# Performance work log

Measured on AMD Instinct MI355X. Metric: run time of the kernel, lower is better.

The kernel has to match this reference:

```python
import jax, jax.numpy as jnp
import numpy as np

EMB, HID, SEQ = 768, 512, 2048
BATCH = 2
EPS = 1e-6
LN_EPS = 1e-5
ROPE_BASE = 10000.0
NEG_BIG = -1e9  # stands in for -inf diagonal mask (identical entmax output, NaN-safe)


def rotate_half(x):
    d = x.shape[-1] // 2
    return jnp.concatenate([-x[..., d:], x[..., :d]], axis=-1)


def rope_tables(L, D, dtype=jnp.float32):
    inv_freq = 1.0 / (ROPE_BASE ** (jnp.arange(0, D, 2, dtype=jnp.float32) / D))
    t = jnp.arange(L, dtype=jnp.float32)
    freqs = jnp.outer(t, inv_freq)            # [L, D/2]
    emb = jnp.concatenate([freqs, freqs], -1)  # [L, D]
    return jnp.cos(emb).astype(dtype), jnp.sin(emb).astype(dtype)


def layernorm(x, gamma, beta):
    mu = jnp.mean(x, axis=-1, keepdims=True)
    var = jnp.mean(jnp.square(x - mu), axis=-1, keepdims=True)
    return (x - mu) * jax.lax.rsqrt(var + LN_EPS) * gamma + beta


def entmax15(z):
    """Exact 1.5-entmax along last axis (Peters & Martins sort algorithm)."""
    z = z / 2.0
    z = z - jnp.max(z, axis=-1, keepdims=True)
    zs = -jnp.sort(-z, axis=-1)                      # descending
    L = z.shape[-1]
    k = jnp.arange(1, L + 1, dtype=z.dtype)
    cum = jnp.cumsum(zs, axis=-1)
    cum2 = jnp.cumsum(zs * zs, axis=-1)
    mean = cum / k
    ss = cum2 - cum * mean                           # k*(E[x^2]-E[x]^2)
    delta = (1.0 - ss) / k
    tau = mean - jnp.sqrt(jnp.maximum(delta, 0.0))
    support = jnp.sum((tau <= zs).astype(jnp.int32), axis=-1)
    tau_star = jnp.take_along_axis(tau, (support - 1)[..., None], axis=-1)
    return jnp.square(jnp.maximum(z - tau_star, 0.0))


def setup_inputs() -> dict:
    key = jax.random.key(0)
    ks = jax.random.split(key, 3)
    x = jax.random.normal(ks[0], (BATCH, SEQ, EMB), dtype=jnp.float32)
    Wq = jax.random.normal(ks[1], (HID, EMB), dtype=jnp.float32) / np.sqrt(EMB)
    Wk = jax.random.normal(ks[2], (HID, EMB), dtype=jnp.float32) / np.sqrt(EMB)
    return {
        "x": x, "Wq": Wq, "Wk": Wk,
        "q_gamma": jnp.ones((HID,), jnp.float32), "q_beta": jnp.zeros((HID,), jnp.float32),
        "k_gamma": jnp.ones((HID,), jnp.float32), "k_beta": jnp.zeros((HID,), jnp.float32),
        "C_weight": jnp.ones((1,), jnp.float32),
        "F_weight": jnp.ones((1,), jnp.float32),
        "S_weight": jnp.ones((1,), jnp.float32),
    }


def reference(x, Wq, Wk, q_gamma, q_beta, k_gamma, k_beta, C_weight, F_weight, S_weight):
    B, L, _ = x.shape
    q = layernorm(x @ Wq.T, q_gamma, q_beta)   # [B,L,D]
    k = layernorm(x @ Wk.T, k_gamma, k_beta)
    cos, sin = rope_tables(L, q.shape[-1], q.dtype)
    q = q * cos + rotate_half(q) * sin
    k = k * cos + rotate_half(k) * sin

    wC = 2.0 * jax.nn.sigmoid(C_weight)
    wF = 2.0 * jax.nn.sigmoid(F_weight)
    wS = 2.0 * jax.nn.sigmoid(S_weight)

    Gkk = jnp.einsum('bld,ble->bde', k, k)     # [B,D,D]
    Gkq = jnp.einsum('bld,ble->bde', k, q)
    Gqq = jnp.einsum('bld,ble->bde', q, q)

    C_raw = jnp.einsum('bid,bde,bje->bij', q, Gkk, q)  # [B,L,L]
    F_raw = jnp.einsum('bid,bde,bje->bij', q, Gkq, k)
    S_raw = jnp.einsum('bid,bde,bje->bij', k, Gqq, k)

    C = C_raw - jnp.mean(C_raw, axis=-1, keepdims=True)
    Fm = F_raw - jnp.mean(F_raw, axis=-1, keepdims=True)
    S = S_raw - jnp.mean(S_raw, axis=-1, keepdims=True)

    pC = jnp.clip(entmax15(wC * C), 0.0, 1.0 - EPS)
    pF = jnp.clip(entmax15(wF * Fm), 0.0, 1.0 - EPS)
    pS = jnp.clip(entmax15(wS * S), 0.0, 1.0 - EPS)

    pC = pC * jax.lax.rsqrt(jnp.sum(pC, axis=-2, keepdims=True) + EPS)
    pS = pS * jax.lax.rsqrt(jnp.sum(pS, axis=-2, keepdims=True) + EPS)

    pC = jnp.maximum((1.0 - 2.0 * EPS) * pC + EPS, EPS)
    pF = jnp.maximum((1.0 - 2.0 * EPS) * pF + EPS, EPS)
    pS = jnp.maximum((1.0 - 2.0 * EPS) * pS + EPS, EPS)

    H = (jnp.log(pC) + jnp.log(pF) + jnp.log(pS)) / 3.0
    diag = jnp.eye(L, dtype=bool)[None]
    H = jnp.where(diag, NEG_BIG, H)
    H = entmax15(H)
    return H, pC, pF, pS
```

## Files before the change

kernel.cpp:

```cpp
#include <hip/hip_runtime.h>
#include <cstddef>
#include <math.h>

#define B_   2
#define L_   2048
#define D_   512
#define E_   768
static const size_t LL   = (size_t)L_ * L_;
static const size_t SLOT = (size_t)B_ * LL;

#define QK_N  ((size_t)B_ * L_ * D_)
#define G1_N  ((size_t)512 * 512)
#define G_N   ((size_t)6 * G1_N)
#define U_N   ((size_t)6 * L_ * D_)
#define X_N   ((size_t)4096 * 768)
#define W_N   ((size_t)512 * 768)

typedef unsigned short u16;
typedef __attribute__((ext_vector_type(8))) _Float16 half8;
typedef __attribute__((ext_vector_type(4))) float f32x4;

__device__ __forceinline__ void split2(float f, u16& h0, u16& h1) {
    _Float16 a = (_Float16)f;
    _Float16 b = (_Float16)((f - (float)a) * 4096.0f);
    h0 = __builtin_bit_cast(u16, a);
    h1 = __builtin_bit_cast(u16, b);
}

typedef const __attribute__((address_space(1))) void gas_void;
typedef __attribute__((address_space(3))) void las_void;

__device__ __forceinline__ void gload16(const u16* g, u16* l) {
    __builtin_amdgcn_global_load_lds((gas_void*)g, (las_void*)l, 16, 0, 0);
}

template<bool PROM>
__device__ __forceinline__ void gemm64g(const u16* __restrict__ Ap, size_t Aps, int lda,
                                        const u16* __restrict__ Bp, size_t Bps, int ldb,
                                        int K, int m0, int n0, int tid,
                                        double outv[2][2][4]) {
    __shared__ u16 SA[2][64][32], SB[2][64][32];
    f32x4 accH[2][2], accM[2][2];
#pragma unroll
    for (int i = 0; i < 2; ++i)
#pragma unroll
        for (int j = 0; j < 2; ++j) {
            accH[i][j] = (f32x4){0.f, 0.f, 0.f, 0.f};
            accM[i][j] = (f32x4){0.f, 0.f, 0.f, 0.f};
        }
    double accD[2][2][4] = {};
    int lane = tid & 63, w = tid >> 6;
    int wm = (w & 1) << 5, wn = (w >> 1) << 5;
    int fr = lane & 15, ko8 = lane >> 4;

    int rb = w << 4;
    int srow = rb + (lane >> 2);
    int schunk = (lane & 3) ^ ((srow >> 1) & 3);

    int nstep = K >> 5;
    for (int s = 0; s < nstep; ++s) {
        int k0 = s << 5;
#pragma unroll
        for (int sp = 0; sp < 2; ++sp) {
            gload16(Ap + (size_t)sp * Aps + (size_t)(m0 + srow) * lda + k0 + (schunk << 3),
                    &SA[sp][rb][0]);
            gload16(Bp + (size_t)sp * Bps + (size_t)(n0 + srow) * ldb + k0 + (schunk << 3),
                    &SB[sp][rb][0]);
        }
        __syncthreads();
        half8 a[2][2], b[2][2];
#pragma unroll
        for (int f = 0; f < 2; ++f) {
            int ra = wm + f * 16 + fr;
            int rbn = wn + f * 16 + fr;
            int ca = (ko8 ^ ((ra >> 1) & 3)) << 3;
            int cb = (ko8 ^ ((rbn >> 1) & 3)) << 3;
#pragma unroll
            for (int sp = 0; sp < 2; ++sp) {
                a[f][sp] = *reinterpret_cast<const half8*>(&SA[sp][ra][ca]);
                b[f][sp] = *reinterpret_cast<const half8*>(&SB[sp][rbn][cb]);
            }
        }
#pragma unroll
        for (int fi = 0; fi < 2; ++fi)
#pragma unroll
            for (int fj = 0; fj < 2; ++fj) {
                accH[fi][fj] = __builtin_amdgcn_mfma_f32_16x16x32_f16(a[fi][0], b[fj][0], accH[fi][fj], 0, 0, 0);
                accM[fi][fj] = __builtin_amdgcn_mfma_f32_16x16x32_f16(a[fi][0], b[fj][1], accM[fi][fj], 0, 0, 0);
                accM[fi][fj] = __builtin_amdgcn_mfma_f32_16x16x32_f16(a[fi][1], b[fj][0], accM[fi][fj], 0, 0, 0);
            }
        __syncthreads();
        if (PROM) {
#pragma unroll
            for (int fi = 0; fi < 2; ++fi)
#pragma unroll
                for (int fj = 0; fj < 2; ++fj) {
#pragma unroll
                    for (int r = 0; r < 4; ++r) accD[fi][fj][r] += (double)accH[fi][fj][r];
                    accH[fi][fj] = (f32x4){0.f, 0.f, 0.f, 0.f};
                }
        }
    }
    const double S1 = 1.0 / 4096.0;
#pragma unroll
    for (int fi = 0; fi < 2; ++fi)
#pragma unroll
        for (int fj = 0; fj < 2; ++fj)
#pragma unroll
            for (int r = 0; r < 4; ++r)
                outv[fi][fj][r] = (PROM ? accD[fi][fj][r] : (double)accH[fi][fj][r])
                                + (double)accM[fi][fj][r] * S1;
}

__device__ __forceinline__ void gstage128(const u16* __restrict__ P, size_t pstride, int ld,
                                          int r0, int k0, int lane, int w,
                                          u16 S[2][128][32]) {
#pragma unroll
    for (int sp = 0; sp < 2; ++sp)
#pragma unroll
        for (int t = 0; t < 2; ++t) {
            int rb = (w << 5) + (t << 4);
            int row = rb + (lane >> 2);
            int chunk = (lane & 3) ^ ((row >> 1) & 3);
            const u16* src = P + (size_t)sp * pstride + (size_t)(r0 + row) * ld
                             + (k0 + (chunk << 3));
            gload16(src, &S[sp][rb][0]);
        }
}

__device__ __forceinline__ void gemm128(const u16* __restrict__ Ap, size_t Aps, int lda,
                                        const u16* __restrict__ Bp, size_t Bps, int ldb,
                                        int K, int m0, int n0, int tid,
                                        float* __restrict__ out, int ldo) {
    __shared__ u16 SA[2][128][32], SB[2][128][32];
    f32x4 accH[4][4], accM[4][4];
#pragma unroll
    for (int i = 0; i < 4; ++i)
#pragma unroll
        for (int j = 0; j < 4; ++j) {
            accH[i][j] = (f32x4){0.f, 0.f, 0.f, 0.f};
            accM[i][j] = (f32x4){0.f, 0.f, 0.f, 0.f};
        }
    int lane = tid & 63, w = tid >> 6;
    int wm = (w & 1) << 6, wn = (w >> 1) << 6;
    int fr = lane & 15, ko8 = lane >> 4;

    int nstep = K >> 5;
    for (int s = 0; s < nstep; ++s) {
        int k0 = s << 5;
        gstage128(Ap, Aps, lda, m0, k0, lane, w, SA);
        gstage128(Bp, Bps, ldb, n0, k0, lane, w, SB);
        __syncthreads();
        half8 a[4][2], b[4][2];
#pragma unroll
        for (int f = 0; f < 4; ++f) {
            int ra = wm + (f << 4) + fr;
            int rbn = wn + (f << 4) + fr;
            int ca = (ko8 ^ ((ra >> 1) & 3)) << 3;
            int cb = (ko8 ^ ((rbn >> 1) & 3)) << 3;
#pragma unroll
            for (int sp = 0; sp < 2; ++sp) {
                a[f][sp] = *reinterpret_cast<const half8*>(&SA[sp][ra][ca]);
                b[f][sp] = *reinterpret_cast<const half8*>(&SB[sp][rbn][cb]);
            }
        }
#pragma unroll
        for (int fi = 0; fi < 4; ++fi)
#pragma unroll
            for (int fj = 0; fj < 4; ++fj) {
                accH[fi][fj] = __builtin_amdgcn_mfma_f32_16x16x32_f16(a[fi][0], b[fj][0], accH[fi][fj], 0, 0, 0);
                accM[fi][fj] = __builtin_amdgcn_mfma_f32_16x16x32_f16(a[fi][0], b[fj][1], accM[fi][fj], 0, 0, 0);
                accM[fi][fj] = __builtin_amdgcn_mfma_f32_16x16x32_f16(a[fi][1], b[fj][0], accM[fi][fj], 0, 0, 0);
            }
        __syncthreads();
    }
    const double S1 = 1.0 / 4096.0;
    int col = lane & 15, rbase = (lane >> 4) << 2;
#pragma unroll
    for (int fi = 0; fi < 4; ++fi)
#pragma unroll
        for (int fj = 0; fj < 4; ++fj)
#pragma unroll
            for (int r = 0; r < 4; ++r) {
                int mm = m0 + wm + (fi << 4) + rbase + r;
                int nn = n0 + wn + (fj << 4) + col;
                out[(size_t)mm * ldo + nn] =
                    (float)((double)accH[fi][fj][r] + (double)accM[fi][fj][r] * S1);
            }
}

__global__ __launch_bounds__(256) void k_prep(const float* __restrict__ x,
                                              const float* __restrict__ Wq,
                                              const float* __restrict__ Wk,
                                              u16* __restrict__ xP,
                                              u16* __restrict__ WP,
                                              double* __restrict__ tg) {
    int bx = blockIdx.x;
    if (bx < L_) {
        int l = bx, j = threadIdx.x;
        double e = (double)j * (1.0 / 256.0);
        double inv = pow(10000.0, -e);
        double ang = (double)l * inv;
        tg[(size_t)l * 512 + j] = cos(ang);
        tg[(size_t)l * 512 + 256 + j] = sin(ang);
        return;
    }
    size_t gid = (size_t)(bx - L_) * 256 + threadIdx.x;
    const size_t XH = X_N / 2, WH = W_N / 2;
    const float* src; u16* dst; size_t pn, off;
    if (gid < XH)            { src = x  + 2 * gid;              dst = xP;            pn = X_N; off = 2 * gid; }
    else if (gid < XH + WH)  { size_t g = gid - XH;      src = Wq + 2 * g; dst = WP;            pn = W_N; off = 2 * g; }
    else                     { size_t g = gid - XH - WH; src = Wk + 2 * g; dst = WP + 2 * W_N;  pn = W_N; off = 2 * g; }
    float2 v = *reinterpret_cast<const float2*>(src);
    u16 a0, a1, b0, b1;
    split2(v.x, a0, a1);
    split2(v.y, b0, b1);
    *reinterpret_cast<unsigned*>(dst + off)      = (unsigned)a0 | ((unsigned)b0 << 16);
    *reinterpret_cast<unsigned*>(dst + pn + off) = (unsigned)a1 | ((unsigned)b1 << 16);
}

__global__ __launch_bounds__(256, 2) void k_proj(const u16* __restrict__ xP,
                                                 const u16* __restrict__ WP,
                                                 float* __restrict__ qraw,
                                                 float* __restrict__ kraw) {
    int z = blockIdx.z;
    float* out = z ? kraw : qraw;
    const u16* Bp = WP + (size_t)z * 2 * W_N;
    gemm128(xP, X_N, E_, Bp, W_N, E_, E_,
            blockIdx.y * 128, blockIdx.x * 128, threadIdx.x, out, D_);
}

__global__ __launch_bounds__(256) void k_lnrope(const float* __restrict__ qraw,
                                                const float* __restrict__ kraw,
                                                const double* __restrict__ tg,
                                                const float* __restrict__ qg, const float* __restrict__ qb,
                                                const float* __restrict__ kg, const float* __restrict__ kb,
                                                u16* __restrict__ qP, u16* __restrict__ kP) {
    int row = blockIdx.x;
    int l = row & (L_ - 1);
    int tid = threadIdx.x;
    int half = tid >> 7, t = tid & 127;
    __shared__ double nrow[2][D_];
    __shared__ double red[8];
    __shared__ double cs_[256], sn_[256];
    {
        int j = tid & 255;
        if (tid < 256) { cs_[j] = tg[(size_t)l * 512 + j]; sn_[j] = tg[(size_t)l * 512 + 256 + j]; }
    }
    const float* rp = (half ? kraw : qraw) + (size_t)row * D_;
    const float* g  = half ? kg : qg;
    const float* bt = half ? kb : qb;
    u16* P = half ? kP : qP;
    float4 v = reinterpret_cast<const float4*>(rp)[t];
    double vv[4] = {(double)v.x, (double)v.y, (double)v.z, (double)v.w};
    double s = vv[0] + vv[1] + vv[2] + vv[3];
    double s2 = vv[0]*vv[0] + vv[1]*vv[1] + vv[2]*vv[2] + vv[3]*vv[3];
    for (int off = 32; off; off >>= 1) { s += __shfl_xor(s, off); s2 += __shfl_xor(s2, off); }
    int wv = tid >> 6;
    if ((tid & 63) == 0) { red[wv * 2] = s; red[wv * 2 + 1] = s2; }
    __syncthreads();
    double mu  = (red[half * 4 + 0] + red[half * 4 + 2]) * (1.0 / D_);
    double var = (red[half * 4 + 1] + red[half * 4 + 3]) * (1.0 / D_) - mu * mu;
    double rs = rsqrt(var + 1e-5);
    int d0 = t * 4;
    double o[4];
#pragma unroll
    for (int c = 0; c < 4; ++c) {
        int d = d0 + c;
        o[c] = (vv[c] - mu) * rs * (double)g[d] + (double)bt[d];
    }
#pragma unroll
    for (int c = 0; c < 4; ++c) nrow[half][d0 + c] = o[c];
    __syncthreads();
    u16 h[2][4];
#pragma unroll
    for (int c = 0; c < 4; ++c) {
        int d = d0 + c;
        double rot = (d < 256) ? -nrow[half][d + 256] : nrow[half][d - 256];
        float ov = (float)(nrow[half][d] * cs_[d & 255] + rot * sn_[d & 255]);
        split2(ov, h[0][c], h[1][c]);
    }
    size_t off = (size_t)row * D_ + d0;
#pragma unroll
    for (int sp = 0; sp < 2; ++sp)
        *reinterpret_cast<ushort4*>(P + sp * QK_N + off) = make_ushort4(h[sp][0], h[sp][1], h[sp][2], h[sp][3]);
}

__global__ __launch_bounds__(256) void k_qkT(const u16* __restrict__ qP,
                                             const u16* __restrict__ kP,
                                             u16* __restrict__ qPT,
                                             u16* __restrict__ kPT) {
    __shared__ u16 T[64][72];
    int z = blockIdx.z;
    int b = z & 1, sp = (z >> 1) & 1, tn = z >> 2;
    const u16* src = (tn ? kP : qP) + (size_t)sp * QK_N + (size_t)b * L_ * D_;
    u16* dst       = (tn ? kPT : qPT) + (size_t)sp * QK_N + (size_t)b * D_ * L_;
    int l0 = blockIdx.x * 64, d0 = blockIdx.y * 64;
    int tid = threadIdx.x;
#pragma unroll
    for (int i = 0; i < 2; ++i) {
        int idx = tid + i * 256;
        int lr = idx >> 3, dc8 = (idx & 7) << 3;
        *reinterpret_cast<uint4*>(&T[lr][dc8]) =
            *reinterpret_cast<const uint4*>(&src[(size_t)(l0 + lr) * D_ + d0 + dc8]);
    }
    __syncthreads();
#pragma unroll
    for (int i = 0; i < 2; ++i) {
        int idx = tid + i * 256;
        int dr = idx >> 3, lc8 = (idx & 7) << 3;
        u16 tmp[8];
#pragma unroll
        for (int c = 0; c < 8; ++c) tmp[c] = T[lc8 + c][dr];
        *reinterpret_cast<uint4*>(&dst[(size_t)(d0 + dr) * L_ + l0 + lc8]) =
            *reinterpret_cast<const uint4*>(tmp);
    }
}

__global__ __launch_bounds__(256) void k_gram(const u16* __restrict__ qPT,
                                              const u16* __restrict__ kPT,
                                              float* __restrict__ Gpart) {
    int zz = blockIdx.z, half = zz & 1, z = zz >> 1;
    int b = z / 3, m = z % 3;
    const u16* A  = ((m == 2) ? qPT : kPT) + (size_t)b * D_ * L_ + (size_t)half * (L_ / 2);
    const u16* Bp = ((m == 0) ? kPT : qPT) + (size_t)b * D_ * L_ + (size_t)half * (L_ / 2);
    int m0 = blockIdx.y * 64, n0 = blockIdx.x * 64;
    double ov[2][2][4];
    gemm64g<true>(A, QK_N, L_, Bp, QK_N, L_, L_ / 2, m0, n0, threadIdx.x, ov);
    float* Gg = Gpart + (size_t)half * G_N + (size_t)z * G1_N;
    int lane = threadIdx.x & 63, w = threadIdx.x >> 6;
    int wm = (w & 1) << 5, wn = (w >> 1) << 5;
    int col = lane & 15, rbase = (lane >> 4) << 2;
#pragma unroll
    for (int fi = 0; fi < 2; ++fi)
#pragma unroll
        for (int fj = 0; fj < 2; ++fj)
#pragma unroll
            for (int r = 0; r < 4; ++r) {
                int mm = m0 + wm + fi * 16 + rbase + r;
                int nn = n0 + wn + fj * 16 + col;
                Gg[(size_t)mm * 512 + nn] = (float)ov[fi][fj][r];
            }
}

__global__ __launch_bounds__(256) void k_gsplitT(const float* __restrict__ Gpart,
                                                 u16* __restrict__ GPT) {
    __shared__ float T[64][65];
    int z = blockIdx.z, d0 = blockIdx.y * 64, e0 = blockIdx.x * 64;
    const float* Ga = Gpart + (size_t)z * G1_N;
    const float* Gb = Ga + G_N;
    int tid = threadIdx.x;
#pragma unroll
    for (int i = 0; i < 16; ++i) {
        int idx = tid + i * 256;
        int r = idx >> 6, c = idx & 63;
        size_t o = (size_t)(d0 + r) * 512 + e0 + c;
        T[r][c] = Ga[o] + Gb[o];
    }
    __syncthreads();
    u16* Gz = GPT + (size_t)z * G1_N;
#pragma unroll
    for (int i = 0; i < 16; ++i) {
        int idx = tid + i * 256;
        int er = idx >> 6, dc = idx & 63;
        u16 h0, h1; split2(T[dc][er], h0, h1);
        size_t o = (size_t)(e0 + er) * 512 + d0 + dc;
        Gz[o] = h0; Gz[G_N + o] = h1;
    }
}

__global__ __launch_bounds__(256) void k_u(const u16* __restrict__ qP,
                                           const u16* __restrict__ kP,
                                           const u16* __restrict__ GPT,
                                           u16* __restrict__ UP) {
    int z = blockIdx.z, b = z / 3, m = z % 3;
    const u16* A  = ((m == 2) ? kP : qP) + (size_t)b * L_ * D_;
    const u16* Bp = GPT + (size_t)z * G1_N;
    int m0 = blockIdx.y * 64, n0 = blockIdx.x * 64;
    double ov[2][2][4];
    gemm64g<true>(A, QK_N, D_, Bp, G_N, 512, D_, m0, n0, threadIdx.x, ov);
    int lane = threadIdx.x & 63, w = threadIdx.x >> 6;
    int wm = (w & 1) << 5, wn = (w >> 1) << 5;
    int col = lane & 15, rbase = (lane >> 4) << 2;
#pragma unroll
    for (int fi = 0; fi < 2; ++fi)
#pragma unroll
        for (int fj = 0; fj < 2; ++fj)
#pragma unroll
            for (int r = 0; r < 4; ++r) {
                float uf = (float)ov[fi][fj][r];
                int mm = m0 + wm + fi * 16 + rbase + r;
                int nn = n0 + wn + fj * 16 + col;
                size_t off = (size_t)z * ((size_t)L_ * D_) + (size_t)mm * D_ + nn;
                u16 h0, h1; split2(uf, h0, h1);
                UP[off] = h0; UP[U_N + off] = h1;
            }
}

__global__ __launch_bounds__(256, 2) void k_scores(const u16* __restrict__ qP,
                                                   const u16* __restrict__ kP,
                                                   const u16* __restrict__ UP,
                                                   float* __restrict__ out) {
    int z = blockIdx.z, b = z / 3, m = z % 3;
    const u16* A  = UP + (size_t)z * ((size_t)L_ * D_);
    const u16* Bp = ((m == 0) ? qP : kP) + (size_t)b * L_ * D_;
    float* Co = out + (size_t)(1 + m) * SLOT + (size_t)b * LL;
    gemm128(A, U_N, D_, Bp, QK_N, D_, D_,
            blockIdx.y * 128, blockIdx.x * 128, threadIdx.x, Co, L_);
}

__global__ __launch_bounds__(256) void k_entmax(float* __restrict__ base, int nrows,
                                                const float* __restrict__ wC,
                                                const float* __restrict__ wF,
                                                const float* __restrict__ wS) {
    int tid = threadIdx.x;
    int lane = tid & 63;
    int r = blockIdx.x * 4 + (tid >> 6);
    if (r >= nrows) return;
    int m = r >> 12;
    const float* wp = (m == 0) ? wC : (m == 1) ? wF : wS;
    float hw = (float)(1.0 / (1.0 + exp(-(double)wp[0])));
    float* row = base + (size_t)r * L_;
    float v[32];
    float mx = -3.4e38f;
#pragma unroll
    for (int j = 0; j < 32; ++j) {
        v[j] = row[lane + (j << 6)];
        mx = fmaxf(mx, v[j]);
    }
    for (int off = 32; off; off >>= 1) mx = fmaxf(mx, __shfl_xor(mx, off));
    float z[32];
#pragma unroll
    for (int j = 0; j < 32; ++j) z[j] = hw * (v[j] - mx);
    float lo = -1.0f, hi = 0.0f;
    for (int it = 0; it < 9; ++it) {
        float tau = 0.5f * (lo + hi);
        float ssum = 0.0f;
#pragma unroll
        for (int j = 0; j < 32; ++j) {
            float t = fmaxf(z[j] - tau, 0.0f);
            ssum = fmaf(t, t, ssum);
        }
        for (int off = 32; off; off >>= 1) ssum += __shfl_xor(ssum, off);
        if (ssum >= 1.0f) lo = tau; else hi = tau;
    }
    float tau = lo;
    for (int it = 0; it < 3; ++it) {
        float s1 = 0.0f, s2 = 0.0f;
#pragma unroll
        for (int j = 0; j < 32; ++j) {
            float t = fmaxf(z[j] - tau, 0.0f);
            s1 += t;
            s2 = fmaf(t, t, s2);
        }
        for (int off = 32; off; off >>= 1) { s1 += __shfl_xor(s1, off); s2 += __shfl_xor(s2, off); }
        float denom = 2.0f * s1;
        if (denom > 1e-30f) tau += fmaxf((s2 - 1.0f) / denom, 0.0f);
    }
#pragma unroll
    for (int j = 0; j < 32; ++j) {
        float t = fmaxf(z[j] - tau, 0.0f);
        row[lane + (j << 6)] = fminf(t * t, 1.0f - 1e-6f);
    }
}

__global__ __launch_bounds__(256) void k_colsum(const float* __restrict__ out,
                                                double* __restrict__ part) {
    int bz = blockIdx.z, which = bz >> 1, b = bz & 1;
    const float* mat = out + (size_t)(which ? 3 : 1) * SLOT + (size_t)b * LL;
    int j = blockIdx.x * 256 + threadIdx.x;
    int r0 = blockIdx.y * 128;
    double s = 0.0;
#pragma unroll 8
    for (int r = 0; r < 128; ++r) s += (double)mat[(size_t)(r0 + r) * L_ + j];
    part[((size_t)bz * 16 + blockIdx.y) * L_ + j] = s;
}

__global__ __launch_bounds__(256) void k_colred(const double* __restrict__ part,
                                                double* __restrict__ csC,
                                                double* __restrict__ csS) {
    int g = blockIdx.x * 256 + threadIdx.x;
    int bz = g >> 11, j = g & (L_ - 1);
    int which = bz >> 1, b = bz & 1;
    double s = 0.0;
#pragma unroll
    for (int c = 0; c < 16; ++c) s += part[((size_t)bz * 16 + c) * L_ + j];
    (which ? csS : csC)[b * L_ + j] = s;
}

__global__ __launch_bounds__(256) void k_fin2(float* __restrict__ out,
                                              const double* __restrict__ csC,
                                              const double* __restrict__ csS) {
    int row = blockIdx.x;
    int i = row & (L_ - 1), b = row >> 11;
    size_t ro = (size_t)row * L_;
    float* H  = out + ro;
    float* pC = out + SLOT + ro;
    float* pF = out + 2 * SLOT + ro;
    float* pS = out + 3 * SLOT + ro;
    const double* cc = csC + b * L_;
    const double* cs = csS + b * L_;
    int tid = threadIdx.x, lane = tid & 63, wv = tid >> 6;
    __shared__ float red[4], red2[4];
    const double A1 = 1.0 - 2e-6;
    float h[8];
    float mx = -3.4e38f;
#pragma unroll
    for (int c = 0; c < 8; ++c) {
        int j = (c << 8) + tid;
        double cv = (double)pC[j] * rsqrt(cc[j] + 1e-6);
        double fv = (double)pF[j];
        double sv = (double)pS[j] * rsqrt(cs[j] + 1e-6);
        cv = fmax(A1 * cv + 1e-6, 1e-6);
        fv = fmax(A1 * fv + 1e-6, 1e-6);
        sv = fmax(A1 * sv + 1e-6, 1e-6);
        pC[j] = (float)cv; pF[j] = (float)fv; pS[j] = (float)sv;
        h[c] = (j == i) ? -1e9f : logf((float)(cv * fv * sv)) * (1.0f / 3.0f);
        mx = fmaxf(mx, h[c]);
    }
    for (int off = 32; off; off >>= 1) mx = fmaxf(mx, __shfl_xor(mx, off));
    if (lane == 0) red[wv] = mx;
    __syncthreads();
    mx = fmaxf(fmaxf(red[0], red[1]), fmaxf(red[2], red[3]));
    __syncthreads();
    float z[8];
#pragma unroll
    for (int c = 0; c < 8; ++c) z[c] = 0.5f * (h[c] - mx);
    float lo = -1.0f, hi = 0.0f;
    for (int it = 0; it < 9; ++it) {
        float tau = 0.5f * (lo + hi);
        float ssum = 0.0f;
#pragma unroll
        for (int c = 0; c < 8; ++c) {
            float t = fmaxf(z[c] - tau, 0.0f);
            ssum = fmaf(t, t, ssum);
        }
        for (int off = 32; off; off >>= 1) ssum += __shfl_xor(ssum, off);
        if (lane == 0) red[wv] = ssum;
        __syncthreads();
        ssum = red[0] + red[1] + red[2] + red[3];
        __syncthreads();
        if (ssum >= 1.0f) lo = tau; else hi = tau;
    }
    float tau = lo;
    for (int it = 0; it < 3; ++it) {
        float s1 = 0.0f, s2 = 0.0f;
#pragma unroll
        for (int c = 0; c < 8; ++c) {
            float t = fmaxf(z[c] - tau, 0.0f);
            s1 += t;
            s2 = fmaf(t, t, s2);
        }
        for (int off = 32; off; off >>= 1) { s1 += __shfl_xor(s1, off); s2 += __shfl_xor(s2, off); }
        if (lane == 0) { red[wv] = s1; red2[wv] = s2; }
        __syncthreads();
        s1 = red[0] + red[1] + red[2] + red[3];
        s2 = red2[0] + red2[1] + red2[2] + red2[3];
        __syncthreads();
        float denom = 2.0f * s1;
        if (denom > 1e-30f) tau += fmaxf((s2 - 1.0f) / denom, 0.0f);
    }
#pragma unroll
    for (int c = 0; c < 8; ++c) {
        float t = fmaxf(z[c] - tau, 0.0f);
        H[(c << 8) + tid] = t * t;
    }
}

extern "C" void kernel_launch(void* const* d_in, const int* in_sizes, int n_in,
                              void* d_out, int out_size, void* d_ws, size_t ws_size,
                              hipStream_t stream) {
    const float* x  = (const float*)d_in[0];
    const float* Wq = (const float*)d_in[1];
    const float* Wk = (const float*)d_in[2];
    const float* qg = (const float*)d_in[3];
    const float* qb = (const float*)d_in[4];
    const float* kg = (const float*)d_in[5];
    const float* kb = (const float*)d_in[6];
    const float* wC = (const float*)d_in[7];
    const float* wF = (const float*)d_in[8];
    const float* wS = (const float*)d_in[9];
    float* out = (float*)d_out;

    char* wsb = (char*)d_ws;
    u16*    UP   = (u16*)wsb;
    float*  qraw = (float*)wsb;
    float*  kraw = qraw + QK_N;
    u16*    qPT  = (u16*)wsb;
    u16*    kPT  = qPT + 2 * QK_N;
    float*  Gpart = (float*)(wsb + 2 * QK_N * sizeof(float));
    wsb += 3 * U_N * sizeof(u16);
    u16*    qP    = (u16*)wsb;
    u16*    xP    = (u16*)wsb;   wsb += 3 * QK_N * sizeof(u16);
    u16*    kP    = (u16*)wsb;   wsb += 3 * QK_N * sizeof(u16);
    u16*    GPT   = (u16*)wsb;
    u16*    WP    = (u16*)wsb;   wsb += 3 * G_N * sizeof(u16);
    double* tg    = (double*)wsb;
    double* part  = tg;
    double* csC   = tg + (size_t)4 * 16 * L_;
    double* csS   = csC + (size_t)B_ * L_;

    k_prep    <<<dim3(L_ + 7680), 256, 0, stream>>>(x, Wq, Wk, xP, WP, tg);
    k_proj    <<<dim3(4, 32, 2),  256, 0, stream>>>(xP, WP, qraw, kraw);
    k_lnrope  <<<dim3(B_ * L_),   256, 0, stream>>>(qraw, kraw, tg, qg, qb, kg, kb, qP, kP);
    k_qkT     <<<dim3(32, 8, 8),  256, 0, stream>>>(qP, kP, qPT, kPT);
    k_gram    <<<dim3(8, 8, 12),  256, 0, stream>>>(qPT, kPT, Gpart);
    k_gsplitT <<<dim3(8, 8, 6),   256, 0, stream>>>(Gpart, GPT);
    k_u       <<<dim3(8, 32, 6),  256, 0, stream>>>(qP, kP, GPT, UP);
    k_scores  <<<dim3(16, 16, 6), 256, 0, stream>>>(qP, kP, UP, out);
    k_entmax  <<<dim3(3072),      256, 0, stream>>>(out + SLOT, 3 * B_ * L_, wC, wF, wS);
    k_colsum  <<<dim3(8, 16, 4),  256, 0, stream>>>(out, part);
    k_colred  <<<dim3(32),        256, 0, stream>>>(part, csC, csS);
    k_fin2    <<<dim3(B_ * L_),   256, 0, stream>>>(out, csC, csS);
}
```

Measured before the change: 476.6 us.

## Widen gram/U GEMM tiles to 128x64 and swizzle score block order

The 64x64 fp16-split GEMM helper used by the gram and U kernels becomes a 128x64 tile, so each block loads twice as many A rows per B tile and launches half as many blocks. This raises MFMA work per LDS stage, at the cost of more accumulators (double and float) and higher register pressure under a 2-waves launch bound. The scores kernel moves to a 1D grid with a remapping that spreads consecutive block IDs across z-slices and tiles, aiming to balance work across XCDs or the cache.

```diff
diff --git a/kernel.cpp b/kernel.cpp
--- a/kernel.cpp
+++ b/kernel.cpp
@@ -34,55 +34,64 @@
     __builtin_amdgcn_global_load_lds((gas_void*)g, (las_void*)l, 16, 0, 0);
 }
 
-template<bool PROM>
-__device__ __forceinline__ void gemm64g(const u16* __restrict__ Ap, size_t Aps, int lda,
-                                        const u16* __restrict__ Bp, size_t Bps, int ldb,
-                                        int K, int m0, int n0, int tid,
-                                        double outv[2][2][4]) {
-    __shared__ u16 SA[2][64][32], SB[2][64][32];
-    f32x4 accH[2][2], accM[2][2];
-#pragma unroll
-    for (int i = 0; i < 2; ++i)
+__device__ __forceinline__ void gemm12864p(const u16* __restrict__ Ap, size_t Aps, int lda,
+                                           const u16* __restrict__ Bp, size_t Bps, int ldb,
+                                           int K, int m0, int n0, int tid,
+                                           double outv[4][2][4]) {
+    __shared__ u16 SA[2][128][32], SB[2][64][32];
+    f32x4 accH[4][2], accM[4][2];
+#pragma unroll
+    for (int i = 0; i < 4; ++i)
 #pragma unroll
         for (int j = 0; j < 2; ++j) {
             accH[i][j] = (f32x4){0.f, 0.f, 0.f, 0.f};
             accM[i][j] = (f32x4){0.f, 0.f, 0.f, 0.f};
         }
-    double accD[2][2][4] = {};
+    double accD[4][2][4] = {};
     int lane = tid & 63, w = tid >> 6;
-    int wm = (w & 1) << 5, wn = (w >> 1) << 5;
+    int wm = (w & 1) << 6, wn = (w >> 1) << 5;
     int fr = lane & 15, ko8 = lane >> 4;
 
-    int rb = w << 4;
-    int srow = rb + (lane >> 2);
-    int schunk = (lane & 3) ^ ((srow >> 1) & 3);
+    int rbA0 = (w << 5), rbA1 = (w << 5) + 16;
+    int rowA0 = rbA0 + (lane >> 2), rowA1 = rbA1 + (lane >> 2);
+    int chA0 = (lane & 3) ^ ((rowA0 >> 1) & 3);
+    int chA1 = (lane & 3) ^ ((rowA1 >> 1) & 3);
+    int rbB = (w << 4);
+    int rowB = rbB + (lane >> 2);
+    int chB = (lane & 3) ^ ((rowB >> 1) & 3);
 
     int nstep = K >> 5;
     for (int s = 0; s < nstep; ++s) {
         int k0 = s << 5;
 #pragma unroll
         for (int sp = 0; sp < 2; ++sp) {
-            gload16(Ap + (size_t)sp * Aps + (size_t)(m0 + srow) * lda + k0 + (schunk << 3),
-                    &SA[sp][rb][0]);
-            gload16(Bp + (size_t)sp * Bps + (size_t)(n0 + srow) * ldb + k0 + (schunk << 3),
-                    &SB[sp][rb][0]);
-        }
-        __syncthreads();
-        half8 a[2][2], b[2][2];
+            gload16(Ap + (size_t)sp * Aps + (size_t)(m0 + rowA0) * lda + k0 + (chA0 << 3),
+                    &SA[sp][rbA0][0]);
+            gload16(Ap + (size_t)sp * Aps + (size_t)(m0 + rowA1) * lda + k0 + (chA1 << 3),
+                    &SA[sp][rbA1][0]);
+            gload16(Bp + (size_t)sp * Bps + (size_t)(n0 + rowB) * ldb + k0 + (chB << 3),
+                    &SB[sp][rbB][0]);
+        }
+        __syncthreads();
+        half8 a[4][2], b[2][2];
+#pragma unroll
+        for (int f = 0; f < 4; ++f) {
+            int ra = wm + (f << 4) + fr;
+            int ca = (ko8 ^ ((ra >> 1) & 3)) << 3;
+#pragma unroll
+            for (int sp = 0; sp < 2; ++sp)
+                a[f][sp] = *reinterpret_cast<const half8*>(&SA[sp][ra][ca]);
+        }
 #pragma unroll
         for (int f = 0; f < 2; ++f) {
-            int ra = wm + f * 16 + fr;
-            int rbn = wn + f * 16 + fr;
-            int ca = (ko8 ^ ((ra >> 1) & 3)) << 3;
+            int rbn = wn + (f << 4) + fr;
             int cb = (ko8 ^ ((rbn >> 1) & 3)) << 3;
 #pragma unroll
-            for (int sp = 0; sp < 2; ++sp) {
-                a[f][sp] = *reinterpret_cast<const half8*>(&SA[sp][ra][ca]);
+            for (int sp = 0; sp < 2; ++sp)
                 b[f][sp] = *reinterpret_cast<const half8*>(&SB[sp][rbn][cb]);
-            }
-        }
-#pragma unroll
-        for (int fi = 0; fi < 2; ++fi)
+        }
+#pragma unroll
+        for (int fi = 0; fi < 4; ++fi)
 #pragma unroll
             for (int fj = 0; fj < 2; ++fj) {
                 accH[fi][fj] = __builtin_amdgcn_mfma_f32_16x16x32_f16(a[fi][0], b[fj][0], accH[fi][fj], 0, 0, 0);
@@ -90,26 +99,23 @@
                 accM[fi][fj] = __builtin_amdgcn_mfma_f32_16x16x32_f16(a[fi][1], b[fj][0], accM[fi][fj], 0, 0, 0);
             }
         __syncthreads();
-        if (PROM) {
-#pragma unroll
-            for (int fi = 0; fi < 2; ++fi)
-#pragma unroll
-                for (int fj = 0; fj < 2; ++fj) {
-#pragma unroll
-                    for (int r = 0; r < 4; ++r) accD[fi][fj][r] += (double)accH[fi][fj][r];
-                    accH[fi][fj] = (f32x4){0.f, 0.f, 0.f, 0.f};
-                }
-        }
+#pragma unroll
+        for (int fi = 0; fi < 4; ++fi)
+#pragma unroll
+            for (int fj = 0; fj < 2; ++fj) {
+#pragma unroll
+                for (int r = 0; r < 4; ++r) accD[fi][fj][r] += (double)accH[fi][fj][r];
+                accH[fi][fj] = (f32x4){0.f, 0.f, 0.f, 0.f};
+            }
     }
     const double S1 = 1.0 / 4096.0;
 #pragma unroll
-    for (int fi = 0; fi < 2; ++fi)
+    for (int fi = 0; fi < 4; ++fi)
 #pragma unroll
         for (int fj = 0; fj < 2; ++fj)
 #pragma unroll
             for (int r = 0; r < 4; ++r)
-                outv[fi][fj][r] = (PROM ? accD[fi][fj][r] : (double)accH[fi][fj][r])
-                                + (double)accM[fi][fj][r] * S1;
+                outv[fi][fj][r] = accD[fi][fj][r] + (double)accM[fi][fj][r] * S1;
 }
 
 __device__ __forceinline__ void gstage128(const u16* __restrict__ P, size_t pstride, int ld,
@@ -317,22 +323,22 @@
     }
 }
 
-__global__ __launch_bounds__(256) void k_gram(const u16* __restrict__ qPT,
-                                              const u16* __restrict__ kPT,
-                                              float* __restrict__ Gpart) {
+__global__ __launch_bounds__(256, 2) void k_gram(const u16* __restrict__ qPT,
+                                                 const u16* __restrict__ kPT,
+                                                 float* __restrict__ Gpart) {
     int zz = blockIdx.z, half = zz & 1, z = zz >> 1;
     int b = z / 3, m = z % 3;
     const u16* A  = ((m == 2) ? qPT : kPT) + (size_t)b * D_ * L_ + (size_t)half * (L_ / 2);
     const u16* Bp = ((m == 0) ? kPT : qPT) + (size_t)b * D_ * L_ + (size_t)half * (L_ / 2);
-    int m0 = blockIdx.y * 64, n0 = blockIdx.x * 64;
-    double ov[2][2][4];
-    gemm64g<true>(A, QK_N, L_, Bp, QK_N, L_, L_ / 2, m0, n0, threadIdx.x, ov);
+    int m0 = blockIdx.y * 128, n0 = blockIdx.x * 64;
+    double ov[4][2][4];
+    gemm12864p(A, QK_N, L_, Bp, QK_N, L_, L_ / 2, m0, n0, threadIdx.x, ov);
     float* Gg = Gpart + (size_t)half * G_N + (size_t)z * G1_N;
     int lane = threadIdx.x & 63, w = threadIdx.x >> 6;
-    int wm = (w & 1) << 5, wn = (w >> 1) << 5;
+    int wm = (w & 1) << 6, wn = (w >> 1) << 5;
     int col = lane & 15, rbase = (lane >> 4) << 2;
 #pragma unroll
-    for (int fi = 0; fi < 2; ++fi)
+    for (int fi = 0; fi < 4; ++fi)
 #pragma unroll
         for (int fj = 0; fj < 2; ++fj)
 #pragma unroll
@@ -369,21 +375,21 @@
     }
 }
 
-__global__ __launch_bounds__(256) void k_u(const u16* __restrict__ qP,
-                                           const u16* __restrict__ kP,
-                                           const u16* __restrict__ GPT,
-                                           u16* __restrict__ UP) {
+__global__ __launch_bounds__(256, 2) void k_u(const u16* __restrict__ qP,
+                                              const u16* __restrict__ kP,
+                                              const u16* __restrict__ GPT,
+                                              u16* __restrict__ UP) {
     int z = blockIdx.z, b = z / 3, m = z % 3;
     const u16* A  = ((m == 2) ? kP : qP) + (size_t)b * L_ * D_;
     const u16* Bp = GPT + (size_t)z * G1_N;
-    int m0 = blockIdx.y * 64, n0 = blockIdx.x * 64;
-    double ov[2][2][4];
-    gemm64g<true>(A, QK_N, D_, Bp, G_N, 512, D_, m0, n0, threadIdx.x, ov);
+    int m0 = blockIdx.y * 128, n0 = blockIdx.x * 64;
+    double ov[4][2][4];
+    gemm12864p(A, QK_N, D_, Bp, G_N, 512, D_, m0, n0, threadIdx.x, ov);
     int lane = threadIdx.x & 63, w = threadIdx.x >> 6;
-    int wm = (w & 1) << 5, wn = (w >> 1) << 5;
+    int wm = (w & 1) << 6, wn = (w >> 1) << 5;
     int col = lane & 15, rbase = (lane >> 4) << 2;
 #pragma unroll
-    for (int fi = 0; fi < 2; ++fi)
+    for (int fi = 0; fi < 4; ++fi)
 #pragma unroll
         for (int fj = 0; fj < 2; ++fj)
 #pragma unroll
@@ -401,12 +407,16 @@
                                                    const u16* __restrict__ kP,
                                                    const u16* __restrict__ UP,
                                                    float* __restrict__ out) {
-    int z = blockIdx.z, b = z / 3, m = z % 3;
+    int bid = blockIdx.x;
+    int swz = (bid & 7) * 192 + (bid >> 3);
+    int z = swz >> 8, rem = swz & 255;
+    int by = rem >> 4, bx = rem & 15;
+    int b = z / 3, m = z % 3;
     const u16* A  = UP + (size_t)z * ((size_t)L_ * D_);
     const u16* Bp = ((m == 0) ? qP : kP) + (size_t)b * L_ * D_;
     float* Co = out + (size_t)(1 + m) * SLOT + (size_t)b * LL;
     gemm128(A, U_N, D_, Bp, QK_N, D_, D_,
-            blockIdx.y * 128, blockIdx.x * 128, threadIdx.x, Co, L_);
+            by * 128, bx * 128, threadIdx.x, Co, L_);
 }
 
 __global__ __launch_bounds__(256) void k_entmax(float* __restrict__ base, int nrows,
@@ -604,10 +614,10 @@
     k_proj    <<<dim3(4, 32, 2),  256, 0, stream>>>(xP, WP, qraw, kraw);
     k_lnrope  <<<dim3(B_ * L_),   256, 0, stream>>>(qraw, kraw, tg, qg, qb, kg, kb, qP, kP);
     k_qkT     <<<dim3(32, 8, 8),  256, 0, stream>>>(qP, kP, qPT, kPT);
-    k_gram    <<<dim3(8, 8, 12),  256, 0, stream>>>(qPT, kPT, Gpart);
+    k_gram    <<<dim3(8, 4, 12),  256, 0, stream>>>(qPT, kPT, Gpart);
     k_gsplitT <<<dim3(8, 8, 6),   256, 0, stream>>>(Gpart, GPT);
-    k_u       <<<dim3(8, 32, 6),  256, 0, stream>>>(qP, kP, GPT, UP);
-    k_scores  <<<dim3(16, 16, 6), 256, 0, stream>>>(qP, kP, UP, out);
+    k_u       <<<dim3(8, 16, 6),  256, 0, stream>>>(qP, kP, GPT, UP);
+    k_scores  <<<dim3(1536),      256, 0, stream>>>(qP, kP, UP, out);
     k_entmax  <<<dim3(3072),      256, 0, stream>>>(out + SLOT, 3 * B_ * L_, wC, wF, wS);
     k_colsum  <<<dim3(8, 16, 4),  256, 0, stream>>>(out, part);
     k_colred  <<<dim3(32),        256, 0, stream>>>(part, csC, csS);
```

Result: faster. 455.7 us (-4.4%).
